# Kernel tuning notes

Measured on AMD Instinct MI355X. Metric: run time of the kernel, lower is better.

## Reference

```python
import jax, jax.numpy as jnp
import numpy as np

EPS = 1e-7
INF = 1e8
SOFT_CENTER_RADIUS = 3.0
TOPK = 13
IOU_WEIGHT = 3.0
NUM_CLASSES = 80
N_PRIORS = 33600
NUM_GT = 256
IMG = 1024.0


def setup_inputs() -> dict:
    key = jax.random.key(0)
    k1, k2, k3, k4, k5, k6, k7 = jax.random.split(key, 7)
    n, g, c = N_PRIORS, NUM_GT, NUM_CLASSES
    pred_scores = jax.random.normal(k1, (n, c), jnp.float32)
    # priors: (cx, cy, stride, stride)
    ctr = jax.random.uniform(k2, (n, 2), jnp.float32) * IMG
    stride = jnp.full((n, 1), 8.0, jnp.float32)
    priors = jnp.concatenate([ctr, stride, stride], axis=-1)
    # predicted boxes, x1y1x2y2
    pwh = jax.random.uniform(k3, (n, 2), jnp.float32) * 96.0 + 8.0
    pctr = jax.random.uniform(k4, (n, 2), jnp.float32) * IMG
    pred_bboxes = jnp.concatenate([pctr - pwh / 2, pctr + pwh / 2], axis=-1)
    # gt boxes, x1y1x2y2
    gwh = jax.random.uniform(k5, (g, 2), jnp.float32) * 192.0 + 16.0
    gctr = jax.random.uniform(k6, (g, 2), jnp.float32) * IMG
    gt_bboxes = jnp.concatenate([gctr - gwh / 2, gctr + gwh / 2], axis=-1)
    gt_labels = jax.random.randint(k7, (g,), 0, c, dtype=jnp.int32).astype(jnp.int64)
    return {"pred_scores": pred_scores, "priors": priors,
            "pred_bboxes": pred_bboxes, "gt_bboxes": gt_bboxes,
            "gt_labels": gt_labels}


def _pairwise_iou(a, b):
    # a: (n,4), b: (g,4), x1y1x2y2 -> (n,g)
    area_a = (a[:, 2] - a[:, 0]) * (a[:, 3] - a[:, 1])
    area_b = (b[:, 2] - b[:, 0]) * (b[:, 3] - b[:, 1])
    lt = jnp.maximum(a[:, None, :2], b[None, :, :2])
    rb = jnp.minimum(a[:, None, 2:], b[None, :, 2:])
    wh = jnp.clip(rb - lt, 0.0, None)
    inter = wh[..., 0] * wh[..., 1]
    union = area_a[:, None] + area_b[None, :] - inter
    return inter / jnp.maximum(union, 1e-6)


def reference(pred_scores, priors, pred_bboxes, gt_bboxes, gt_labels):
    n, g = pred_bboxes.shape[0], gt_bboxes.shape[0]
    gt_labels = gt_labels.astype(jnp.int32)

    # ---- find_inside_points (box_dim == 4) ----
    pts = priors[:, :2]                                   # (n,2)
    lt = pts[:, None, :] - gt_bboxes[None, :, :2]
    rb = gt_bboxes[None, :, 2:] - pts[:, None, :]
    is_in_gts = jnp.min(jnp.concatenate([lt, rb], -1), -1) > 0   # (n,g)
    pad_bbox_flag = gt_bboxes.sum(-1) > 0                        # (g,)
    is_in_gts = is_in_gts & pad_bbox_flag[None, :]
    valid_mask = jnp.any(is_in_gts, -1)                          # (n,)

    # ---- soft center prior ----
    gt_center = (gt_bboxes[:, :2] + gt_bboxes[:, 2:]) * 0.5      # (g,2)
    dist = jnp.sqrt(((pts[:, None, :] - gt_center[None, :, :]) ** 2).sum(-1))
    dist = dist / priors[:, 2:3]                                 # / stride
    dist = dist * valid_mask[:, None].astype(dist.dtype)
    soft_center_prior = jnp.power(10.0, dist - SOFT_CENTER_RADIUS)

    # ---- iou cost ----
    ious = _pairwise_iou(pred_bboxes, gt_bboxes)                 # (n,g)
    iou_cost = -jnp.log(ious + EPS) * IOU_WEIGHT

    # ---- soft classification cost (BCE-with-logits, iou targets) ----
    logits = pred_scores[:, gt_labels]                           # (n,g)
    scale = jnp.abs(ious - jax.nn.sigmoid(logits)) ** 2
    bce = jnp.maximum(logits, 0) - logits * ious + jnp.log1p(jnp.exp(-jnp.abs(logits)))
    cost = bce * scale + iou_cost + soft_center_prior
    cost = jnp.where(valid_mask[:, None], cost, INF)

    # ---- dynamic k matching (vectorized over GTs) ----
    K = min(TOPK, n)
    topk_ious, _ = jax.lax.top_k(ious.T, K)                      # (g,K)
    dynamic_ks = jnp.clip(topk_ious.sum(-1).astype(jnp.int32), 1, None)  # (g,)
    _, cand_idx = jax.lax.top_k(-cost.T, K)                      # (g,K) lowest-cost priors per gt
    sel = (jnp.arange(K)[None, :] < dynamic_ks[:, None]).astype(jnp.float32)
    matching = jnp.zeros((g, n), jnp.float32).at[
        jnp.arange(g)[:, None], cand_idx].set(sel).T             # (n,g)

    # resolve priors matched to multiple gts -> keep min-cost gt
    multi = matching.sum(-1) > 1
    onehot_min = jax.nn.one_hot(jnp.argmin(cost, -1), g, dtype=jnp.float32)
    matching = jnp.where(multi[:, None], onehot_min, matching)

    fg = matching.sum(-1) > 0
    matched_gt_inds = jnp.argmax(matching, -1)                   # (n,)
    matched_pred_ious = (matching * ious).sum(-1)                # (n,)

    final = fg & valid_mask
    assigned_gt_inds = jnp.where(final, matched_gt_inds + 1, 0)
    assigned_labels = jnp.where(final, gt_labels[matched_gt_inds], -1)
    max_overlaps = jnp.where(final, matched_pred_ious, -INF)
    return assigned_gt_inds, max_overlaps, assigned_labels
```

## Files before the change

### kernel.cpp

```cpp
#include <hip/hip_runtime.h>
#include <cstdint>

#define NPRI 33600
#define NGT  256
#define NCLS 80
#define KTOP 13
#define INF_F 1.0e8f
#define EPS_F 1e-7f
#define L10 3.3219280948873623f
#define SLC  4
#define SLEN (NPRI / SLC)
#define SCN_T 512
#define NW8 (SCN_T / 64)
#define NIT  ((SLEN + SCN_T - 1) / SCN_T)
#define CAPI 1536
#define CAPC 512
#define RFIX 5.5f
#define PREP_BLKS ((NPRI + 255) / 256)
#define NEGINF __int_as_float(0xff800000)

typedef unsigned long long u64;

__device__ __forceinline__ int get_label(const void* p, int j, int is64) {
    if (is64) return (int)((const long long*)p)[j];
    return ((const int*)p)[j];
}

__device__ __forceinline__ float wave_max_bc_f32(float v) {
    #pragma unroll
    for (int off = 32; off > 0; off >>= 1) v = fmaxf(v, __shfl_down(v, off, 64));
    return __int_as_float(__builtin_amdgcn_readfirstlane(__float_as_int(v)));
}
__device__ __forceinline__ u64 wave_min_bc_u64(u64 v) {
    #pragma unroll
    for (int off = 32; off > 0; off >>= 1) { u64 o = __shfl_down(v, off, 64); v = (o < v) ? o : v; }
    unsigned lo = (unsigned)__builtin_amdgcn_readfirstlane((int)(v & 0xffffffffull));
    unsigned hi = (unsigned)__builtin_amdgcn_readfirstlane((int)(v >> 32));
    return (((u64)hi) << 32) | lo;
}
template<int NSL>
__device__ __forceinline__ void wave_merge_max13_f32(float (&l)[NSL], float* dst, int lane) {
    int p = 0;
    for (int r = 0; r < KTOP; ++r) {
        float cur = NEGINF;
        #pragma unroll
        for (int s = 0; s < NSL; ++s) if (s == p) cur = l[NSL - 1 - s];
        float bm = wave_max_bc_f32(cur);
        u64 m = __ballot(cur == bm && bm != NEGINF);
        int first = __ffsll(m) - 1;
        if (lane == first) p++;
        if (lane == 0) dst[r] = bm;
    }
}
template<int NSL>
__device__ __forceinline__ void wave_merge_minN(u64 (&l)[NSL], u64* dst, int lane) {
    int p = 0;
    for (int r = 0; r < KTOP; ++r) {
        u64 cur = ~0ull;
        #pragma unroll
        for (int s = 0; s < NSL; ++s) if (s == p) cur = l[s];
        u64 bm = wave_min_bc_u64(cur);
        if (cur == bm && bm != ~0ull) p++;
        if (lane == 0) dst[r] = bm;
    }
}

__device__ __forceinline__ float iou_exact(float4 pb, float areap, float gx1, float gy1,
                                           float gx2, float gy2, float areag) {
    float iw = fmaxf(fminf(pb.z, gx2) - fmaxf(pb.x, gx1), 0.0f);
    float ih = fmaxf(fminf(pb.w, gy2) - fmaxf(pb.y, gy1), 0.0f);
    float inter = iw * ih;
    return inter / fmaxf(areap + areag - inter, 1e-6f);
}
__device__ __forceinline__ float cost_exact(float4 p2, float gcx, float gcy,
                                            float l, float iou) {
    float dx = p2.x - gcx, dy = p2.y - gcy;
    float dist = sqrtf(dx * dx + dy * dy) / p2.z;
    float soft = exp2f((dist - 3.0f) * L10);
    float sig = 1.0f / (1.0f + expf(-l));
    float dd = iou - sig;
    float bce = fmaxf(l, 0.0f) - l * iou + log1pf(expf(-fabsf(l)));
    float iouc = -logf(iou + EPS_F) * 3.0f;
    return bce * (dd * dd) + iouc + soft;
}

__global__ __launch_bounds__(256) void k_prep(
        const float* __restrict__ priors, const float* __restrict__ gt,
        const void* labels, const float* __restrict__ pboxes,
        float4* __restrict__ pbp,
        int* count, int* firstgt, int* flag, int* nmulti) {
    __shared__ float4 gbox[NGT];
    __shared__ int    gpad[NGT];
    __shared__ int    bad;
    const int tid = threadIdx.x;
    const int b = blockIdx.x;
    if (b == 0 && tid == 0) { bad = 0; *nmulti = 0; }
    {
        float4 bx = ((const float4*)gt)[tid];
        gbox[tid] = bx;
        gpad[tid] = ((bx.x + bx.y + bx.z + bx.w) > 0.0f) ? 1 : 0;
    }
    __syncthreads();
    if (b == 0 && tid < 128) {
        long long v = ((const long long*)labels)[tid];
        if (v < 0 || v >= NCLS) atomicOr(&bad, 1);
    }
    int i = b * 256 + tid;
    if (i < NPRI) {
        count[i] = 0; firstgt[i] = NGT;
        float4 pr = ((const float4*)priors)[i];
        float px = pr.x, py = pr.y;
        int v = 0;
        for (int j = 0; j < NGT; ++j) {
            float4 bx = gbox[j];
            float m = fminf(fminf(px - bx.x, py - bx.y), fminf(bx.z - px, bx.w - py));
            if (m > 0.0f && gpad[j]) { v = 1; break; }
        }
        pbp[2 * i]     = ((const float4*)pboxes)[i];
        pbp[2 * i + 1] = make_float4(px, py, pr.z, v ? 1.0f : 0.0f);
    }
    if (b == 0) {
        __syncthreads();
        if (tid == 0) *flag = bad ? 0 : 1;
    }
}

__global__ __launch_bounds__(SCN_T) void k_scan(
        const float* __restrict__ scores,
        const float4* __restrict__ pbp,
        const float* __restrict__ gt, const void* labels, const int* flag,
        float* __restrict__ part_iou, u64* __restrict__ part_cost) {
    const int tid = threadIdx.x, lane = tid & 63, wid = tid >> 6;
    const int j = blockIdx.x, slice = blockIdx.y;
    const int base = slice * SLEN;
    const int lim = base + SLEN;
    const int is64 = *flag;

    const float4 gb = ((const float4*)gt)[j];
    const float gx1 = gb.x, gy1 = gb.y, gx2 = gb.z, gy2 = gb.w;
    const float areag = (gx2 - gx1) * (gy2 - gy1);
    const float gcx = (gx1 + gx2) * 0.5f, gcy = (gy1 + gy2) * 0.5f;
    const int lab = get_label(labels, j, is64);

    __shared__ int s_ni, s_nc, s_mode;
    __shared__ float s_dmax;
    __shared__ float liou[CAPI];
    __shared__ int lcost[CAPC];
    __shared__ float wiof[NW8 * KTOP];
    __shared__ u64 wco[NW8 * KTOP];
    __shared__ u64 csel[KTOP];
    if (tid == 0) { s_ni = 0; s_nc = 0; }
    __syncthreads();

    {
        const int i0 = base + tid;
        int ia1 = i0 + SCN_T; ia1 = (ia1 < lim) ? ia1 : i0;
        float4 pb_c = pbp[2 * i0],  p2_c = pbp[2 * i0 + 1];
        float4 pb_n = pbp[2 * ia1], p2_n = pbp[2 * ia1 + 1];
        for (int it = 0; it < NIT; ++it) {
            int i = i0 + it * SCN_T;
            int ipre = i + 2 * SCN_T;
            int ic = (ipre < lim) ? ipre : i0;
            float4 pb_p = pbp[2 * ic];
            float4 p2_p = pbp[2 * ic + 1];

            bool inb = (i < lim);
            float iou = 0.0f;
            bool pc = false;
            if (inb) {
                float areap = (pb_c.z - pb_c.x) * (pb_c.w - pb_c.y);
                float iw = fmaxf(fminf(pb_c.z, gx2) - fmaxf(pb_c.x, gx1), 0.0f);
                float ih = fmaxf(fminf(pb_c.w, gy2) - fmaxf(pb_c.y, gy1), 0.0f);
                float inter = iw * ih;
                iou = inter / fmaxf(areap + areag - inter, 1e-6f);
                if (p2_c.w != 0.0f) {
                    float dx = p2_c.x - gcx, dy = p2_c.y - gcy;
                    float rad = p2_c.z * RFIX;
                    pc = (dx * dx + dy * dy <= rad * rad * (1.0f + 1e-5f));
                }
            }
            bool pi = inb && (iou > 0.0f);
            u64 mi = __ballot(pi);
            if (mi) {
                int lead = __ffsll(mi) - 1;
                int cnt = __popcll(mi);
                int bs = 0;
                if (lane == lead) bs = atomicAdd(&s_ni, cnt);
                bs = __shfl(bs, lead, 64);
                if (pi) {
                    int p = bs + __popcll(mi & ((1ull << lane) - 1ull));
                    if (p < CAPI) liou[p] = iou;
                }
            }
            u64 mc = __ballot(pc);
            if (mc) {
                int lead = __ffsll(mc) - 1;
                int cnt = __popcll(mc);
                int bs = 0;
                if (lane == lead) bs = atomicAdd(&s_nc, cnt);
                bs = __shfl(bs, lead, 64);
                if (pc) {
                    int p = bs + __popcll(mc & ((1ull << lane) - 1ull));
                    if (p < CAPC) lcost[p] = i;
                }
            }
            pb_c = pb_n; p2_c = p2_n;
            pb_n = pb_p; p2_n = p2_p;
        }
    }
    __syncthreads();
    const int ni = s_ni, nc = s_nc;
    const int ncc = (nc < CAPC) ? nc : CAPC;
    const bool fI = (ni > CAPI);

    if (wid == 0) {
        u64 lf[KTOP];
        #pragma unroll
        for (int s = 0; s < KTOP; ++s) lf[s] = ~0ull;
        for (int k = lane; k < ncc; k += 64) {
            int i = lcost[k];
            float4 pb = pbp[2 * i];
            float4 p2 = pbp[2 * i + 1];
            float areap = (pb.z - pb.x) * (pb.w - pb.y);
            float iou = iou_exact(pb, areap, gx1, gy1, gx2, gy2, areag);
            float ec = cost_exact(p2, gcx, gcy, scores[(size_t)i * NCLS + lab], iou);
            u64 ck = (((u64)__float_as_uint(ec)) << 32) | (unsigned)i;
            if (ck < lf[KTOP - 1]) {
                lf[KTOP - 1] = ck;
                #pragma unroll
                for (int s = KTOP - 1; s > 0; --s)
                    if (lf[s] < lf[s - 1]) { u64 t = lf[s]; lf[s] = lf[s - 1]; lf[s - 1] = t; }
            }
        }
        wave_merge_minN<KTOP>(lf, csel, lane);
        if (lane == 0) {
            u64 tk = csel[KTOP - 1];
            int mode; float dmax = 0.0f;
            if (tk == ~0ull) mode = 2;
            else {
                float tau = __uint_as_float((unsigned)(tk >> 32));
                if (!(tau < 9.0e7f)) mode = 2;
                else {
                    dmax = 3.0f + __log2f(tau + 1e-5f) * (1.0f / L10) + 4e-3f;
                    mode = (dmax > RFIX || nc > CAPC) ? 1 : 0;
                }
            }
            s_mode = mode; s_dmax = dmax;
        }
    } else if (wid == 1 && !fI) {
        float lf[KTOP];
        #pragma unroll
        for (int s = 0; s < KTOP; ++s) lf[s] = NEGINF;
        int nn = (ni < CAPI) ? ni : CAPI;
        for (int k = lane; k < nn; k += 64) {
            float v = liou[k];
            if (v > lf[0]) {
                lf[0] = v;
                #pragma unroll
                for (int s = 0; s < KTOP - 1; ++s)
                    if (lf[s] > lf[s + 1]) { float t = lf[s]; lf[s] = lf[s + 1]; lf[s + 1] = t; }
            }
        }
        wave_merge_max13_f32<KTOP>(lf, part_iou + ((size_t)j * SLC + slice) * KTOP, lane);
    }
    __syncthreads();

    if (fI) {
        float lf[KTOP];
        #pragma unroll
        for (int s = 0; s < KTOP; ++s) lf[s] = NEGINF;
        for (int i = base + tid; i < lim; i += SCN_T) {
            float4 pb = pbp[2 * i];
            float areap = (pb.z - pb.x) * (pb.w - pb.y);
            float iou = iou_exact(pb, areap, gx1, gy1, gx2, gy2, areag);
            if (iou > lf[0]) {
                lf[0] = iou;
                #pragma unroll
                for (int s = 0; s < KTOP - 1; ++s)
                    if (lf[s] > lf[s + 1]) { float t = lf[s]; lf[s] = lf[s + 1]; lf[s + 1] = t; }
            }
        }
        wave_merge_max13_f32<KTOP>(lf, &wiof[wid * KTOP], lane);
        __syncthreads();
        if (wid == 0) {
            float* dpi = part_iou + ((size_t)j * SLC + slice) * KTOP;
            int p = 0;
            for (int r = 0; r < KTOP; ++r) {
                float cur = (lane < NW8 && p < KTOP) ? wiof[lane * KTOP + p] : NEGINF;
                float bm = wave_max_bc_f32(cur);
                u64 m = __ballot(cur == bm && bm != NEGINF);
                int first = __ffsll(m) - 1;
                if (lane == first) p++;
                if (lane == 0) dpi[r] = bm;
            }
        }
        __syncthreads();
    }

    int mode = s_mode;
    if (mode == 1) {
        const float dmax = s_dmax;
        if (tid == 0) s_nc = 0;
        __syncthreads();
        for (int i = base + tid; i < lim; i += SCN_T) {
            float4 p2 = pbp[2 * i + 1];
            if (p2.w != 0.0f) {
                float dx = p2.x - gcx, dy = p2.y - gcy;
                float rad = p2.z * dmax;
                if (dx * dx + dy * dy <= rad * rad * (1.0f + 1e-5f)) {
                    int p = atomicAdd(&s_nc, 1);
                    if (p < CAPC) lcost[p] = i;
                }
            }
        }
        __syncthreads();
        int nc2 = s_nc;
        if (nc2 <= CAPC) {
            if (wid == 0) {
                u64 lf[KTOP];
                #pragma unroll
                for (int s = 0; s < KTOP; ++s) lf[s] = ~0ull;
                for (int k = lane; k < nc2; k += 64) {
                    int i = lcost[k];
                    float4 pb = pbp[2 * i];
                    float4 p2 = pbp[2 * i + 1];
                    float areap = (pb.z - pb.x) * (pb.w - pb.y);
                    float iou = iou_exact(pb, areap, gx1, gy1, gx2, gy2, areag);
                    float ec = cost_exact(p2, gcx, gcy, scores[(size_t)i * NCLS + lab], iou);
                    u64 ck = (((u64)__float_as_uint(ec)) << 32) | (unsigned)i;
                    if (ck < lf[KTOP - 1]) {
                        lf[KTOP - 1] = ck;
                        #pragma unroll
                        for (int s = KTOP - 1; s > 0; --s)
                            if (lf[s] < lf[s - 1]) { u64 t = lf[s]; lf[s] = lf[s - 1]; lf[s - 1] = t; }
                    }
                }
                wave_merge_minN<KTOP>(lf, csel, lane);
            }
        } else {
            mode = 2;
        }
        __syncthreads();
    }
    if (mode == 2) {
        u64 lf[KTOP];
        #pragma unroll
        for (int s = 0; s < KTOP; ++s) lf[s] = ~0ull;
        for (int i = base + tid; i < lim; i += SCN_T) {
            float4 pb = pbp[2 * i];
            float4 p2 = pbp[2 * i + 1];
            float areap = (pb.z - pb.x) * (pb.w - pb.y);
            float iou = iou_exact(pb, areap, gx1, gy1, gx2, gy2, areag);
            float ec = INF_F;
            if (p2.w != 0.0f) ec = cost_exact(p2, gcx, gcy, scores[(size_t)i * NCLS + lab], iou);
            u64 k2 = (((u64)__float_as_uint(ec)) << 32) | (unsigned)i;
            if (k2 < lf[KTOP - 1]) {
                lf[KTOP - 1] = k2;
                #pragma unroll
                for (int s = KTOP - 1; s > 0; --s)
                    if (lf[s] < lf[s - 1]) { u64 t = lf[s]; lf[s] = lf[s - 1]; lf[s - 1] = t; }
            }
        }
        wave_merge_minN<KTOP>(lf, &wco[wid * KTOP], lane);
        __syncthreads();
        if (wid == 0) {
            int p = 0;
            for (int r = 0; r < KTOP; ++r) {
                u64 cur = (lane < NW8 && p < KTOP) ? wco[lane * KTOP + p] : ~0ull;
                u64 bm = wave_min_bc_u64(cur);
                if (cur == bm && bm != ~0ull) p++;
                if (lane == 0) csel[r] = bm;
            }
        }
        __syncthreads();
    }
    if (tid < KTOP) {
        u64* dpc = part_cost + ((size_t)j * SLC + slice) * KTOP;
        dpc[tid] = csel[tid];
    }
}

__global__ __launch_bounds__(64) void k_merge(
        const float* __restrict__ part_iou, const u64* __restrict__ part_cost,
        int* count, int* firstgt) {
    const int j = blockIdx.x;
    const int lane = threadIdx.x;
    float vi = (lane < SLC * KTOP) ? part_iou[(size_t)j * SLC * KTOP + lane] : NEGINF;
    float tsum = 0.0f;
    for (int r = 0; r < KTOP; ++r) {
        float bm = wave_max_bc_f32(vi);
        u64 m = __ballot(vi == bm && bm != NEGINF);
        int first = __ffsll(m) - 1;
        if (lane == first) vi = NEGINF;
        tsum += (bm == NEGINF) ? 0.0f : bm;
    }
    int ks = (int)tsum;
    if (ks < 1) ks = 1;
    u64 kc = (lane < SLC * KTOP) ? part_cost[(size_t)j * SLC * KTOP + lane] : ~0ull;
    u64 mine = ~0ull;
    for (int r = 0; r < KTOP; ++r) {
        u64 bm = wave_min_bc_u64(kc);
        if (kc == bm && bm != ~0ull) kc = ~0ull;
        if (lane == r) mine = bm;
    }
    if (lane < KTOP && lane < ks && mine != ~0ull) {
        int idx = (int)(unsigned)(mine & 0xFFFFFFFFull);
        atomicAdd(&count[idx], 1);
        atomicMin(&firstgt[idx], j);
    }
}

__global__ __launch_bounds__(256) void k_assign(
        const float4* __restrict__ pbp, const float* __restrict__ gt,
        const void* labels, const int* flag,
        const int* __restrict__ count, const int* __restrict__ firstgt,
        int* nmulti, int* mlist, float* __restrict__ out) {
    __shared__ float4 gbox[NGT];
    __shared__ int glab[NGT];
    __shared__ float gareas[NGT];
    int tid = threadIdx.x;
    int is64 = *flag;
    {
        float4 b = ((const float4*)gt)[tid];
        gbox[tid] = b;
        glab[tid] = get_label(labels, tid, is64);
        gareas[tid] = (b.z - b.x) * (b.w - b.y);
    }
    __syncthreads();
    int i = blockIdx.x * 256 + tid;
    if (i >= NPRI) return;
    float4 p2 = pbp[2 * i + 1];
    int v = (p2.w != 0.0f) ? 1 : 0;
    int c = count[i];
    float o0 = 0.0f, o1 = -INF_F, o2 = -1.0f;
    if (v && c == 1) {
        int j = firstgt[i];
        float4 pb = pbp[2 * i];
        float areap = (pb.z - pb.x) * (pb.w - pb.y);
        float4 g = gbox[j];
        float iw = fmaxf(fminf(pb.z, g.z) - fmaxf(pb.x, g.x), 0.0f);
        float ih = fmaxf(fminf(pb.w, g.w) - fmaxf(pb.y, g.y), 0.0f);
        float inter = iw * ih;
        float iou = inter / fmaxf(areap + gareas[j] - inter, 1e-6f);
        o0 = (float)(j + 1); o1 = iou; o2 = (float)glab[j];
    } else if (v && c > 1) {
        int pos = atomicAdd(nmulti, 1);
        mlist[pos] = i;
    }
    out[i] = o0;
    out[NPRI + i] = o1;
    out[2 * NPRI + i] = o2;
}

__global__ __launch_bounds__(256) void k_multi(
        const float* __restrict__ scores,
        const float4* __restrict__ pbp, const float* __restrict__ gt,
        const void* labels, const int* flag,
        const int* __restrict__ nmulti, const int* __restrict__ mlist,
        float* __restrict__ out) {
    __shared__ float4 gbox[NGT];
    __shared__ int glab[NGT];
    __shared__ float gcxs[NGT], gcys[NGT], gareas[NGT];
    __shared__ u64 red4[4];
    const int tid = threadIdx.x;
    const int is64 = *flag;
    {
        float4 b = ((const float4*)gt)[tid];
        gbox[tid] = b;
        glab[tid] = get_label(labels, tid, is64);
        gcxs[tid] = (b.x + b.z) * 0.5f;
        gcys[tid] = (b.y + b.w) * 0.5f;
        gareas[tid] = (b.z - b.x) * (b.w - b.y);
    }
    __syncthreads();
    const int nm = *nmulti;
    const int j = tid;
    for (int m = blockIdx.x; m < nm; m += gridDim.x) {
        const int i = mlist[m];
        float4 pb = pbp[2 * i];
        float4 p2 = pbp[2 * i + 1];
        float areap = (pb.z - pb.x) * (pb.w - pb.y);

        float4 g = gbox[j];
        float iw = fmaxf(fminf(pb.z, g.z) - fmaxf(pb.x, g.x), 0.0f);
        float ih = fmaxf(fminf(pb.w, g.w) - fmaxf(pb.y, g.y), 0.0f);
        float inter = iw * ih;
        float iou = inter / fmaxf(areap + gareas[j] - inter, 1e-6f);
        float dx = p2.x - gcxs[j], dy = p2.y - gcys[j];
        float dist = sqrtf(dx * dx + dy * dy) / p2.z;
        float soft = exp2f((dist - 3.0f) * L10);
        float l = scores[(size_t)i * NCLS + glab[j]];
        float sig = 1.0f / (1.0f + expf(-l));
        float dd = iou - sig;
        float bce = fmaxf(l, 0.0f) - l * iou + log1pf(expf(-fabsf(l)));
        float cost = bce * (dd * dd) + (-logf(iou + EPS_F) * 3.0f) + soft;

        u64 key = (((u64)__float_as_uint(cost)) << 32) | (unsigned)j;
        u64 v = key;
        #pragma unroll
        for (int off = 32; off > 0; off >>= 1) {
            u64 o = __shfl_down(v, off, 64);
            v = (o < v) ? o : v;
        }
        if ((tid & 63) == 0) red4[tid >> 6] = v;
        __syncthreads();
        u64 best = red4[0];
        #pragma unroll
        for (int q = 1; q < 4; ++q) best = (red4[q] < best) ? red4[q] : best;
        if (key == best) {
            out[i] = (float)(j + 1);
            out[NPRI + i] = iou;
            out[2 * NPRI + i] = (float)glab[j];
        }
        __syncthreads();
    }
}

extern "C" void kernel_launch(void* const* d_in, const int* in_sizes, int n_in,
                              void* d_out, int out_size, void* d_ws, size_t ws_size,
                              hipStream_t stream) {
    const float* scores = (const float*)d_in[0];
    const float* priors = (const float*)d_in[1];
    const float* pboxes = (const float*)d_in[2];
    const float* gt     = (const float*)d_in[3];
    const void*  labels = d_in[4];
    float* out = (float*)d_out;

    char* ws = (char*)d_ws;
    size_t off = 0;
    auto alloc = [&](size_t bytes) { size_t o = off; off = (off + bytes + 255) & ~(size_t)255; return o; };
    int*    flag     = (int*)(ws + alloc(4));
    int*    nmulti   = (int*)(ws + alloc(4));
    int*    count    = (int*)(ws + alloc((size_t)NPRI * 4));
    int*    firstgt  = (int*)(ws + alloc((size_t)NPRI * 4));
    int*    mlist    = (int*)(ws + alloc((size_t)NPRI * 4));
    float*  part_iou = (float*)(ws + alloc((size_t)NGT * SLC * KTOP * 4));
    u64*    part_cost= (u64*)(ws + alloc((size_t)NGT * SLC * KTOP * 8));
    float4* pbp      = (float4*)(ws + alloc((size_t)NPRI * 32));
    (void)ws_size;

    hipLaunchKernelGGL(k_prep, dim3(PREP_BLKS), dim3(256), 0, stream,
                       priors, gt, labels, pboxes, pbp, count, firstgt, flag, nmulti);
    hipLaunchKernelGGL(k_scan, dim3(NGT, SLC), dim3(SCN_T), 0, stream,
                       scores, pbp, gt, labels, flag, part_iou, part_cost);
    hipLaunchKernelGGL(k_merge, dim3(NGT), dim3(64), 0, stream,
                       part_iou, part_cost, count, firstgt);
    hipLaunchKernelGGL(k_assign, dim3((NPRI + 255) / 256), dim3(256), 0, stream,
                       pbp, gt, labels, flag, count, firstgt, nmulti, mlist, out);
    hipLaunchKernelGGL(k_multi, dim3(256), dim3(256), 0, stream,
                       scores, pbp, gt, labels, flag, nmulti, mlist, out);
}
```

Before: 149.2 us.

## Fuse merge into scan via last-block counter and multi resolve into assign

Removes the separate k_merge launch: the last k_scan block to finish for each GT, detected with an atomic slice counter and threadfences, performs the top-k merge and the count/firstgt updates. The k_multi kernel is folded into k_assign, where each block collects its own multi-matched priors in a shared list and resolves them in place, dropping the global nmulti/mlist workspace. This cuts two kernel launches and their gaps, but serializes the multi resolution inside the assign blocks that contain such priors. It also assumes at most 256 multi-matched priors per block, which holds because each block has 256 threads.

```diff
diff --git a/kernel.cpp b/kernel.cpp
--- a/kernel.cpp
+++ b/kernel.cpp
@@ -88,13 +88,14 @@
         const float* __restrict__ priors, const float* __restrict__ gt,
         const void* labels, const float* __restrict__ pboxes,
         float4* __restrict__ pbp,
-        int* count, int* firstgt, int* flag, int* nmulti) {
+        int* count, int* firstgt, int* flag, int* slice_done) {
     __shared__ float4 gbox[NGT];
     __shared__ int    gpad[NGT];
     __shared__ int    bad;
     const int tid = threadIdx.x;
     const int b = blockIdx.x;
-    if (b == 0 && tid == 0) { bad = 0; *nmulti = 0; }
+    if (b == 0 && tid == 0) bad = 0;
+    if (b == 0) slice_done[tid] = 0;
     {
         float4 bx = ((const float4*)gt)[tid];
         gbox[tid] = bx;
@@ -129,7 +130,8 @@
         const float* __restrict__ scores,
         const float4* __restrict__ pbp,
         const float* __restrict__ gt, const void* labels, const int* flag,
-        float* __restrict__ part_iou, u64* __restrict__ part_cost) {
+        float* __restrict__ part_iou, u64* __restrict__ part_cost,
+        int* count, int* firstgt, int* slice_done) {
     const int tid = threadIdx.x, lane = tid & 63, wid = tid >> 6;
     const int j = blockIdx.x, slice = blockIdx.y;
     const int base = slice * SLEN;
@@ -142,7 +144,7 @@
     const float gcx = (gx1 + gx2) * 0.5f, gcy = (gy1 + gy2) * 0.5f;
     const int lab = get_label(labels, j, is64);
 
-    __shared__ int s_ni, s_nc, s_mode;
+    __shared__ int s_ni, s_nc, s_mode, s_last;
     __shared__ float s_dmax;
     __shared__ float liou[CAPI];
     __shared__ int lcost[CAPC];
@@ -378,89 +380,53 @@
         u64* dpc = part_cost + ((size_t)j * SLC + slice) * KTOP;
         dpc[tid] = csel[tid];
     }
-}
-
-__global__ __launch_bounds__(64) void k_merge(
-        const float* __restrict__ part_iou, const u64* __restrict__ part_cost,
-        int* count, int* firstgt) {
-    const int j = blockIdx.x;
-    const int lane = threadIdx.x;
-    float vi = (lane < SLC * KTOP) ? part_iou[(size_t)j * SLC * KTOP + lane] : NEGINF;
-    float tsum = 0.0f;
-    for (int r = 0; r < KTOP; ++r) {
-        float bm = wave_max_bc_f32(vi);
-        u64 m = __ballot(vi == bm && bm != NEGINF);
-        int first = __ffsll(m) - 1;
-        if (lane == first) vi = NEGINF;
-        tsum += (bm == NEGINF) ? 0.0f : bm;
-    }
-    int ks = (int)tsum;
-    if (ks < 1) ks = 1;
-    u64 kc = (lane < SLC * KTOP) ? part_cost[(size_t)j * SLC * KTOP + lane] : ~0ull;
-    u64 mine = ~0ull;
-    for (int r = 0; r < KTOP; ++r) {
-        u64 bm = wave_min_bc_u64(kc);
-        if (kc == bm && bm != ~0ull) kc = ~0ull;
-        if (lane == r) mine = bm;
-    }
-    if (lane < KTOP && lane < ks && mine != ~0ull) {
-        int idx = (int)(unsigned)(mine & 0xFFFFFFFFull);
-        atomicAdd(&count[idx], 1);
-        atomicMin(&firstgt[idx], j);
+
+    __syncthreads();
+    if (tid == 0) {
+        __threadfence();
+        s_last = (atomicAdd(&slice_done[j], 1) == SLC - 1) ? 1 : 0;
+    }
+    __syncthreads();
+    if (s_last && wid == 0) {
+        __threadfence();
+        const int l = lane;
+        float vi = (l < SLC * KTOP) ? part_iou[(size_t)j * SLC * KTOP + l] : NEGINF;
+        float tsum = 0.0f;
+        for (int r = 0; r < KTOP; ++r) {
+            float bm = wave_max_bc_f32(vi);
+            u64 mmask = __ballot(vi == bm && bm != NEGINF);
+            int first = __ffsll(mmask) - 1;
+            if (l == first) vi = NEGINF;
+            tsum += (bm == NEGINF) ? 0.0f : bm;
+        }
+        int ks = (int)tsum;
+        if (ks < 1) ks = 1;
+        u64 kc = (l < SLC * KTOP) ? part_cost[(size_t)j * SLC * KTOP + l] : ~0ull;
+        u64 mine = ~0ull;
+        for (int r = 0; r < KTOP; ++r) {
+            u64 bm = wave_min_bc_u64(kc);
+            if (kc == bm && bm != ~0ull) kc = ~0ull;
+            if (l == r) mine = bm;
+        }
+        if (l < KTOP && l < ks && mine != ~0ull) {
+            int idx = (int)(unsigned)(mine & 0xFFFFFFFFull);
+            atomicAdd(&count[idx], 1);
+            atomicMin(&firstgt[idx], j);
+        }
     }
 }
 
 __global__ __launch_bounds__(256) void k_assign(
+        const float* __restrict__ scores,
         const float4* __restrict__ pbp, const float* __restrict__ gt,
         const void* labels, const int* flag,
         const int* __restrict__ count, const int* __restrict__ firstgt,
-        int* nmulti, int* mlist, float* __restrict__ out) {
-    __shared__ float4 gbox[NGT];
-    __shared__ int glab[NGT];
-    __shared__ float gareas[NGT];
-    int tid = threadIdx.x;
-    int is64 = *flag;
-    {
-        float4 b = ((const float4*)gt)[tid];
-        gbox[tid] = b;
-        glab[tid] = get_label(labels, tid, is64);
-        gareas[tid] = (b.z - b.x) * (b.w - b.y);
-    }
-    __syncthreads();
-    int i = blockIdx.x * 256 + tid;
-    if (i >= NPRI) return;
-    float4 p2 = pbp[2 * i + 1];
-    int v = (p2.w != 0.0f) ? 1 : 0;
-    int c = count[i];
-    float o0 = 0.0f, o1 = -INF_F, o2 = -1.0f;
-    if (v && c == 1) {
-        int j = firstgt[i];
-        float4 pb = pbp[2 * i];
-        float areap = (pb.z - pb.x) * (pb.w - pb.y);
-        float4 g = gbox[j];
-        float iw = fmaxf(fminf(pb.z, g.z) - fmaxf(pb.x, g.x), 0.0f);
-        float ih = fmaxf(fminf(pb.w, g.w) - fmaxf(pb.y, g.y), 0.0f);
-        float inter = iw * ih;
-        float iou = inter / fmaxf(areap + gareas[j] - inter, 1e-6f);
-        o0 = (float)(j + 1); o1 = iou; o2 = (float)glab[j];
-    } else if (v && c > 1) {
-        int pos = atomicAdd(nmulti, 1);
-        mlist[pos] = i;
-    }
-    out[i] = o0;
-    out[NPRI + i] = o1;
-    out[2 * NPRI + i] = o2;
-}
-
-__global__ __launch_bounds__(256) void k_multi(
-        const float* __restrict__ scores,
-        const float4* __restrict__ pbp, const float* __restrict__ gt,
-        const void* labels, const int* flag,
-        const int* __restrict__ nmulti, const int* __restrict__ mlist,
         float* __restrict__ out) {
     __shared__ float4 gbox[NGT];
     __shared__ int glab[NGT];
     __shared__ float gcxs[NGT], gcys[NGT], gareas[NGT];
+    __shared__ int s_nm;
+    __shared__ int s_mlist[256];
     __shared__ u64 red4[4];
     const int tid = threadIdx.x;
     const int is64 = *flag;
@@ -472,13 +438,40 @@
         gcys[tid] = (b.y + b.w) * 0.5f;
         gareas[tid] = (b.z - b.x) * (b.w - b.y);
     }
-    __syncthreads();
-    const int nm = *nmulti;
+    if (tid == 0) s_nm = 0;
+    __syncthreads();
+    const int i = blockIdx.x * 256 + tid;
+    const bool act = (i < NPRI);
+    if (act) {
+        float4 p2 = pbp[2 * i + 1];
+        int v = (p2.w != 0.0f) ? 1 : 0;
+        int c = count[i];
+        float o0 = 0.0f, o1 = -INF_F, o2 = -1.0f;
+        if (v && c == 1) {
+            int j = firstgt[i];
+            float4 pb = pbp[2 * i];
+            float areap = (pb.z - pb.x) * (pb.w - pb.y);
+            float4 g = gbox[j];
+            float iw = fmaxf(fminf(pb.z, g.z) - fmaxf(pb.x, g.x), 0.0f);
+            float ih = fmaxf(fminf(pb.w, g.w) - fmaxf(pb.y, g.y), 0.0f);
+            float inter = iw * ih;
+            float iou = inter / fmaxf(areap + gareas[j] - inter, 1e-6f);
+            o0 = (float)(j + 1); o1 = iou; o2 = (float)glab[j];
+        } else if (v && c > 1) {
+            int p = atomicAdd(&s_nm, 1);
+            s_mlist[p] = i;
+        }
+        out[i] = o0;
+        out[NPRI + i] = o1;
+        out[2 * NPRI + i] = o2;
+    }
+    __syncthreads();
+    const int nm = s_nm;
     const int j = tid;
-    for (int m = blockIdx.x; m < nm; m += gridDim.x) {
-        const int i = mlist[m];
-        float4 pb = pbp[2 * i];
-        float4 p2 = pbp[2 * i + 1];
+    for (int m = 0; m < nm; ++m) {
+        const int ii = s_mlist[m];
+        float4 pb = pbp[2 * ii];
+        float4 p2 = pbp[2 * ii + 1];
         float areap = (pb.z - pb.x) * (pb.w - pb.y);
 
         float4 g = gbox[j];
@@ -489,7 +482,7 @@
         float dx = p2.x - gcxs[j], dy = p2.y - gcys[j];
         float dist = sqrtf(dx * dx + dy * dy) / p2.z;
         float soft = exp2f((dist - 3.0f) * L10);
-        float l = scores[(size_t)i * NCLS + glab[j]];
+        float l = scores[(size_t)ii * NCLS + glab[j]];
         float sig = 1.0f / (1.0f + expf(-l));
         float dd = iou - sig;
         float bce = fmaxf(l, 0.0f) - l * iou + log1pf(expf(-fabsf(l)));
@@ -508,9 +501,9 @@
         #pragma unroll
         for (int q = 1; q < 4; ++q) best = (red4[q] < best) ? red4[q] : best;
         if (key == best) {
-            out[i] = (float)(j + 1);
-            out[NPRI + i] = iou;
-            out[2 * NPRI + i] = (float)glab[j];
+            out[ii] = (float)(j + 1);
+            out[NPRI + ii] = iou;
+            out[2 * NPRI + ii] = (float)glab[j];
         }
         __syncthreads();
     }
@@ -529,24 +522,20 @@
     char* ws = (char*)d_ws;
     size_t off = 0;
     auto alloc = [&](size_t bytes) { size_t o = off; off = (off + bytes + 255) & ~(size_t)255; return o; };
-    int*    flag     = (int*)(ws + alloc(4));
-    int*    nmulti   = (int*)(ws + alloc(4));
-    int*    count    = (int*)(ws + alloc((size_t)NPRI * 4));
-    int*    firstgt  = (int*)(ws + alloc((size_t)NPRI * 4));
-    int*    mlist    = (int*)(ws + alloc((size_t)NPRI * 4));
-    float*  part_iou = (float*)(ws + alloc((size_t)NGT * SLC * KTOP * 4));
-    u64*    part_cost= (u64*)(ws + alloc((size_t)NGT * SLC * KTOP * 8));
-    float4* pbp      = (float4*)(ws + alloc((size_t)NPRI * 32));
+    int*    flag      = (int*)(ws + alloc(4));
+    int*    slice_done= (int*)(ws + alloc((size_t)NGT * 4));
+    int*    count     = (int*)(ws + alloc((size_t)NPRI * 4));
+    int*    firstgt   = (int*)(ws + alloc((size_t)NPRI * 4));
+    float*  part_iou  = (float*)(ws + alloc((size_t)NGT * SLC * KTOP * 4));
+    u64*    part_cost = (u64*)(ws + alloc((size_t)NGT * SLC * KTOP * 8));
+    float4* pbp       = (float4*)(ws + alloc((size_t)NPRI * 32));
     (void)ws_size;
 
     hipLaunchKernelGGL(k_prep, dim3(PREP_BLKS), dim3(256), 0, stream,
-                       priors, gt, labels, pboxes, pbp, count, firstgt, flag, nmulti);
+                       priors, gt, labels, pboxes, pbp, count, firstgt, flag, slice_done);
     hipLaunchKernelGGL(k_scan, dim3(NGT, SLC), dim3(SCN_T), 0, stream,
-                       scores, pbp, gt, labels, flag, part_iou, part_cost);
-    hipLaunchKernelGGL(k_merge, dim3(NGT), dim3(64), 0, stream,
-                       part_iou, part_cost, count, firstgt);
+                       scores, pbp, gt, labels, flag, part_iou, part_cost,
+                       count, firstgt, slice_done);
     hipLaunchKernelGGL(k_assign, dim3((NPRI + 255) / 256), dim3(256), 0, stream,
-                       pbp, gt, labels, flag, count, firstgt, nmulti, mlist, out);
-    hipLaunchKernelGGL(k_multi, dim3(256), dim3(256), 0, stream,
-                       scores, pbp, gt, labels, flag, nmulti, mlist, out);
-}
+                       scores, pbp, gt, labels, flag, count, firstgt, out);
+}
```

After: 168.9 us. 1.13x slower.
